# Kernel tuning notes

Hardware: AMD Instinct MI355X
Metric: run time of the kernel (lower is better)

## Reference

```python
import jax, jax.numpy as jnp
import numpy as np

A = 512   # input channels
B = 32    # number of capsule types
H4 = 16   # h*h pose dims per capsule


def setup_inputs() -> dict:
    key = jax.random.key(0)
    k1, k2, k3, k4, k5 = jax.random.split(key, 5)
    # Input feature map [N, A, H, W]
    x = jax.random.normal(k1, (64, A, 32, 32), dtype=jnp.float32)
    # Fused weights: B parallel 1x1 convs concatenated along out-channel dim.
    # Pose convs: B x Conv2d(A -> 16, k=1) -> [B*16, A]; activation convs: B x Conv2d(A -> 1) -> [B, A]
    bound = 1.0 / np.sqrt(A)  # PyTorch Conv2d default init range
    W_pose = jax.random.uniform(k2, (B * H4, A), minval=-bound, maxval=bound, dtype=jnp.float32)
    b_pose = jax.random.uniform(k3, (B * H4,), minval=-bound, maxval=bound, dtype=jnp.float32)
    W_act = jax.random.uniform(k4, (B, A), minval=-bound, maxval=bound, dtype=jnp.float32)
    b_act = jax.random.uniform(k5, (B,), minval=-bound, maxval=bound, dtype=jnp.float32)
    return {"x": x, "W_pose": W_pose, "b_pose": b_pose, "W_act": W_act, "b_act": b_act}


def reference(x, W_pose, b_pose, W_act, b_act):
    # 1x1 conv == channel contraction; fuse all 2*B tiny convs into two GEMMs.
    # poses: [N, B*16, H, W]
    poses = jnp.einsum('nahw,oa->nohw', x, W_pose) + b_pose[None, :, None, None]
    # activations: sigmoid([N, B, H, W])
    activations = jax.nn.sigmoid(jnp.einsum('nahw,oa->nohw', x, W_act) + b_act[None, :, None, None])
    return poses, activations
```

## Files before the change

kernel.cpp:

```cpp
#include <hip/hip_runtime.h>
#include <hip/hip_bf16.h>


typedef __attribute__((ext_vector_type(8))) short short8;
typedef __attribute__((ext_vector_type(4))) float f32x4;

#define A_CH   512
#define HW     1024
#define N_B    64
#define O_POSE 512
#define O_ACT  32
#define O_TOT  544
#define O_PAD  640
#define TO     128
#define TM     128
#define BK     32
#define NIT    (A_CH / BK)

__device__ __forceinline__ unsigned pk(float lo, float hi) {
    __hip_bfloat162 h = __float22bfloat162_rn(make_float2(lo, hi));
    return *reinterpret_cast<unsigned*>(&h);
}

__device__ __forceinline__ void glds16(const void* g, void* l) {
    __builtin_amdgcn_global_load_lds(
        (const __attribute__((address_space(1))) unsigned*)g,
        (__attribute__((address_space(3))) unsigned*)l, 16, 0, 0);
}

__global__ __launch_bounds__(256) void prep_w(const float* __restrict__ Wp,
                                              const float* __restrict__ Wa,
                                              unsigned short* __restrict__ Wb) {
    const int r = blockIdx.x;
    const int c = threadIdx.x * 2;
    float2 v = make_float2(0.f, 0.f);
    if (r < O_POSE)     v = *(const float2*)(Wp + (size_t)r * A_CH + c);
    else if (r < O_TOT) v = *(const float2*)(Wa + (size_t)(r - O_POSE) * A_CH + c);
    __hip_bfloat162 h = __float22bfloat162_rn(v);
    *(unsigned*)(Wb + (size_t)r * A_CH + c) = *reinterpret_cast<unsigned*>(&h);
}

__global__ __launch_bounds__(512, 4) void caps_gemm(
    const float* __restrict__ x,
    const unsigned short* __restrict__ Wb,
    const float* __restrict__ bp,
    const float* __restrict__ ba,
    float* __restrict__ out)
{
    __shared__ __align__(16) short ldsA[3][TO * BK];
    __shared__ __align__(16) short ldsB[2][TM * BK];

    const int tid = threadIdx.x;

    const int lin  = blockIdx.x;
    const int xcd  = lin & 7;
    const int slot = lin >> 3;
    const int ob   = slot % 5;
    const int mnid = (slot / 5) * 8 + xcd;
    const int m0   = (mnid & 7) * TM;
    const int n    = mnid >> 3;
    const int o0   = ob * TO;

    const unsigned short* asrc =
        Wb + (size_t)(o0 + (tid >> 2)) * A_CH + (((tid & 3) ^ ((tid >> 3) & 3)) * 8);

    const int sm = tid & 127;
    const int kg = tid >> 7;
    const float* sbase = x + (size_t)n * A_CH * HW + m0 + sm + (size_t)(kg * 8) * HW;
    const int xwr = sm * BK + ((kg ^ ((sm >> 1) & 3)) * 8);

    float xr[2][8];

    const int lane = tid & 63;
    const int w    = tid >> 6;
    const int wo   = (w >> 2) * 64;
    const int wm   = (w & 3) * 32;
    const int l16  = lane & 15;
    const int g    = lane >> 4;

    f32x4 acc[4][2] = {};

    glds16(asrc, &ldsA[0][tid * 8]);
#pragma unroll
    for (int j = 0; j < 8; ++j) xr[0][j] = sbase[(size_t)j * HW];
    asm volatile("" ::: "memory");
    glds16(asrc + BK, &ldsA[1][tid * 8]);
#pragma unroll
    for (int j = 0; j < 8; ++j) xr[1][j] = sbase[(size_t)(BK + j) * HW];

    asm volatile("s_waitcnt vmcnt(9)" ::: "memory");
    {
        short8 v;
#pragma unroll
        for (int j = 0; j < 4; ++j)
            ((unsigned*)&v)[j] = pk(xr[0][2 * j], xr[0][2 * j + 1]);
        *(short8*)&ldsB[0][xwr] = v;
    }
    asm volatile("s_waitcnt lgkmcnt(0)\n\ts_barrier" ::: "memory");

#pragma unroll
    for (int it = 0; it < NIT; ++it) {
        if (it + 2 < NIT) {
            glds16(asrc + (it + 2) * BK, &ldsA[(it + 2) % 3][tid * 8]);
#pragma unroll
            for (int j = 0; j < 8; ++j)
                xr[it & 1][j] = sbase[(size_t)((it + 2) * BK + j) * HW];
        }
        short8 aF[4], bF[2];
#pragma unroll
        for (int f = 0; f < 4; ++f) {
            const int r = wo + f * 16 + l16;
            aF[f] = *(const short8*)&ldsA[it % 3][r * BK + ((g ^ ((r >> 1) & 3)) * 8)];
        }
#pragma unroll
        for (int f = 0; f < 2; ++f) {
            const int c = wm + f * 16 + l16;
            bF[f] = *(const short8*)&ldsB[it & 1][c * BK + ((g ^ ((c >> 1) & 3)) * 8)];
        }
#pragma unroll
        for (int fo = 0; fo < 4; ++fo)
#pragma unroll
            for (int fm = 0; fm < 2; ++fm)
                acc[fo][fm] = __builtin_amdgcn_mfma_f32_16x16x32_bf16(
                    aF[fo], bF[fm], acc[fo][fm], 0, 0, 0);
        if (it + 1 < NIT) {
            if (it + 2 < NIT)
                asm volatile("s_waitcnt vmcnt(9)" ::: "memory");
            else
                asm volatile("s_waitcnt vmcnt(0)" ::: "memory");
            short8 v;
#pragma unroll
            for (int j = 0; j < 4; ++j)
                ((unsigned*)&v)[j] = pk(xr[(it + 1) & 1][2 * j], xr[(it + 1) & 1][2 * j + 1]);
            *(short8*)&ldsB[(it + 1) & 1][xwr] = v;
            asm volatile("s_waitcnt lgkmcnt(0)\n\ts_barrier" ::: "memory");
        }
    }

    float* actOut = out + (size_t)N_B * O_POSE * HW;
    const size_t poseN = (size_t)n * O_POSE * HW;
    const size_t actN  = (size_t)n * O_ACT * HW;
#pragma unroll
    for (int fo = 0; fo < 4; ++fo) {
#pragma unroll
        for (int i = 0; i < 4; ++i) {
            const int R = o0 + wo + fo * 16 + g * 4 + i;
            if (R >= O_TOT) continue;
            if (R < O_POSE) {
                const float bias = bp[R];
#pragma unroll
                for (int fm = 0; fm < 2; ++fm) {
                    const int cc = m0 + wm + fm * 16 + l16;
                    __builtin_nontemporal_store(acc[fo][fm][i] + bias,
                                                &out[poseN + (size_t)R * HW + cc]);
                }
            } else {
                const float bias = ba[R - O_POSE];
#pragma unroll
                for (int fm = 0; fm < 2; ++fm) {
                    const int cc = m0 + wm + fm * 16 + l16;
                    const float v = acc[fo][fm][i] + bias;
                    __builtin_nontemporal_store(1.0f / (1.0f + __expf(-v)),
                                                &actOut[actN + (size_t)(R - O_POSE) * HW + cc]);
                }
            }
        }
    }
}

extern "C" void kernel_launch(void* const* d_in, const int* in_sizes, int n_in,
                              void* d_out, int out_size, void* d_ws, size_t ws_size,
                              hipStream_t stream) {
    (void)in_sizes; (void)n_in; (void)out_size; (void)ws_size;
    const float* x  = (const float*)d_in[0];
    const float* Wp = (const float*)d_in[1];
    const float* bp = (const float*)d_in[2];
    const float* Wa = (const float*)d_in[3];
    const float* ba = (const float*)d_in[4];
    unsigned short* Wb = (unsigned short*)d_ws;

    prep_w<<<dim3(O_PAD), dim3(256), 0, stream>>>(Wp, Wa, Wb);
    caps_gemm<<<dim3(8 * 5 * N_B), dim3(512), 0, stream>>>(x, Wb, bp, ba, (float*)d_out);
}
```

Measured before the change: 296.4 us.

## Halve workgroup size with 64x64 warp tiles and double-buffered weight staging

```diff
diff --git a/kernel.cpp b/kernel.cpp
--- a/kernel.cpp
+++ b/kernel.cpp
@@ -40,14 +40,14 @@
     *(unsigned*)(Wb + (size_t)r * A_CH + c) = *reinterpret_cast<unsigned*>(&h);
 }
 
-__global__ __launch_bounds__(512, 4) void caps_gemm(
+__global__ __launch_bounds__(256, 3) void caps_gemm(
     const float* __restrict__ x,
     const unsigned short* __restrict__ Wb,
     const float* __restrict__ bp,
     const float* __restrict__ ba,
     float* __restrict__ out)
 {
-    __shared__ __align__(16) short ldsA[3][TO * BK];
+    __shared__ __align__(16) short ldsA[2][TO * BK];
     __shared__ __align__(16) short ldsB[2][TM * BK];
 
     const int tid = threadIdx.x;
@@ -61,79 +61,106 @@
     const int n    = mnid >> 3;
     const int o0   = ob * TO;
 
-    const unsigned short* asrc =
-        Wb + (size_t)(o0 + (tid >> 2)) * A_CH + (((tid & 3) ^ ((tid >> 3) & 3)) * 8);
-
-    const int sm = tid & 127;
-    const int kg = tid >> 7;
-    const float* sbase = x + (size_t)n * A_CH * HW + m0 + sm + (size_t)(kg * 8) * HW;
-    const int xwr = sm * BK + ((kg ^ ((sm >> 1) & 3)) * 8);
-
-    float xr[2][8];
+    const int arow = tid >> 2;
+    const int aslt = tid & 3;
+    const unsigned short* asrc1 =
+        Wb + (size_t)(o0 + arow) * A_CH + ((aslt ^ ((arow >> 1) & 3)) * 8);
+    const unsigned short* asrc2 = asrc1 + (size_t)64 * A_CH;
+
+    const int sm  = tid & 127;
+    const int kg  = tid >> 7;
+    const float* sbase = x + (size_t)n * A_CH * HW + m0 + sm;
+    const int swz = (sm >> 1) & 3;
+    const int wr0 = sm * BK + (((2 * kg)     ^ swz) * 8);
+    const int wr1 = sm * BK + (((2 * kg + 1) ^ swz) * 8);
+
+    float xr[2][16];
 
     const int lane = tid & 63;
     const int w    = tid >> 6;
-    const int wo   = (w >> 2) * 64;
-    const int wm   = (w & 3) * 32;
+    const int wo   = (w >> 1) * 64;
+    const int wm   = (w & 1) * 64;
     const int l16  = lane & 15;
     const int g    = lane >> 4;
 
-    f32x4 acc[4][2] = {};
-
-    glds16(asrc, &ldsA[0][tid * 8]);
-#pragma unroll
-    for (int j = 0; j < 8; ++j) xr[0][j] = sbase[(size_t)j * HW];
+    const unsigned baseA = (unsigned)(uintptr_t)&ldsA[0][0];
+    const unsigned baseB = (unsigned)(uintptr_t)&ldsB[0][0];
+    unsigned aoff[4], boff[4];
+#pragma unroll
+    for (int f = 0; f < 4; ++f) {
+        const int r = wo + f * 16 + l16;
+        aoff[f] = baseA + (unsigned)(r * BK + ((g ^ ((r >> 1) & 3)) * 8)) * 2u;
+        const int c = wm + f * 16 + l16;
+        boff[f] = baseB + (unsigned)(c * BK + ((g ^ ((c >> 1) & 3)) * 8)) * 2u;
+    }
+
+    f32x4 acc[4][4] = {};
+
+    glds16(asrc1, &ldsA[0][tid * 8]);
+    glds16(asrc2, &ldsA[0][2048 + tid * 8]);
     asm volatile("" ::: "memory");
-    glds16(asrc + BK, &ldsA[1][tid * 8]);
-#pragma unroll
-    for (int j = 0; j < 8; ++j) xr[1][j] = sbase[(size_t)(BK + j) * HW];
-
-    asm volatile("s_waitcnt vmcnt(9)" ::: "memory");
+#pragma unroll
+    for (int j = 0; j < 16; ++j) xr[0][j] = sbase[(size_t)(kg * 16 + j) * HW];
+    asm volatile("" ::: "memory");
+#pragma unroll
+    for (int j = 0; j < 16; ++j) xr[1][j] = sbase[(size_t)(BK + kg * 16 + j) * HW];
+    asm volatile("s_waitcnt vmcnt(16)" ::: "memory");
     {
-        short8 v;
-#pragma unroll
-        for (int j = 0; j < 4; ++j)
-            ((unsigned*)&v)[j] = pk(xr[0][2 * j], xr[0][2 * j + 1]);
-        *(short8*)&ldsB[0][xwr] = v;
-    }
-    asm volatile("s_waitcnt lgkmcnt(0)\n\ts_barrier" ::: "memory");
+        short8 v0, v1;
+#pragma unroll
+        for (int j = 0; j < 4; ++j) {
+            ((unsigned*)&v0)[j] = pk(xr[0][2 * j],     xr[0][2 * j + 1]);
+            ((unsigned*)&v1)[j] = pk(xr[0][8 + 2 * j], xr[0][9 + 2 * j]);
+        }
+        *(short8*)&ldsB[0][wr0] = v0;
+        *(short8*)&ldsB[0][wr1] = v1;
+    }
+    asm volatile("s_waitcnt lgkmcnt(0)\ns_barrier" ::: "memory");
 
 #pragma unroll
     for (int it = 0; it < NIT; ++it) {
+        const int cur = it & 1;
+        if (it + 1 < NIT) {
+            glds16(asrc1 + (it + 1) * BK, &ldsA[cur ^ 1][tid * 8]);
+            glds16(asrc2 + (it + 1) * BK, &ldsA[cur ^ 1][2048 + tid * 8]);
+            asm volatile("" ::: "memory");
+        }
         if (it + 2 < NIT) {
-            glds16(asrc + (it + 2) * BK, &ldsA[(it + 2) % 3][tid * 8]);
-#pragma unroll
-            for (int j = 0; j < 8; ++j)
-                xr[it & 1][j] = sbase[(size_t)((it + 2) * BK + j) * HW];
-        }
-        short8 aF[4], bF[2];
-#pragma unroll
-        for (int f = 0; f < 4; ++f) {
-            const int r = wo + f * 16 + l16;
-            aF[f] = *(const short8*)&ldsA[it % 3][r * BK + ((g ^ ((r >> 1) & 3)) * 8)];
-        }
-#pragma unroll
-        for (int f = 0; f < 2; ++f) {
-            const int c = wm + f * 16 + l16;
-            bF[f] = *(const short8*)&ldsB[it & 1][c * BK + ((g ^ ((c >> 1) & 3)) * 8)];
-        }
+#pragma unroll
+            for (int j = 0; j < 16; ++j)
+                xr[cur][j] = sbase[(size_t)((it + 2) * BK + kg * 16 + j) * HW];
+        }
+        short8 aF[4], bF[4];
+#pragma unroll
+        for (int f = 0; f < 4; ++f)
+            asm volatile("ds_read_b128 %0, %1" : "=v"(aF[f]) : "v"(aoff[f] + cur * 8192u));
+#pragma unroll
+        for (int f = 0; f < 4; ++f)
+            asm volatile("ds_read_b128 %0, %1" : "=v"(bF[f]) : "v"(boff[f] + cur * 8192u));
+        asm volatile("s_waitcnt lgkmcnt(0)" ::: "memory");
+        __builtin_amdgcn_sched_barrier(0);
 #pragma unroll
         for (int fo = 0; fo < 4; ++fo)
 #pragma unroll
-            for (int fm = 0; fm < 2; ++fm)
+            for (int fm = 0; fm < 4; ++fm)
                 acc[fo][fm] = __builtin_amdgcn_mfma_f32_16x16x32_bf16(
                     aF[fo], bF[fm], acc[fo][fm], 0, 0, 0);
         if (it + 1 < NIT) {
+            if (it + 2 < NIT) asm volatile("s_waitcnt vmcnt(18)" ::: "memory");
+            else              asm volatile("s_waitcnt vmcnt(2)"  ::: "memory");
+            const int b = cur ^ 1;
+            short8 v0, v1;
+#pragma unroll
+            for (int j = 0; j < 4; ++j) {
+                ((unsigned*)&v0)[j] = pk(xr[b][2 * j],     xr[b][2 * j + 1]);
+                ((unsigned*)&v1)[j] = pk(xr[b][8 + 2 * j], xr[b][9 + 2 * j]);
+            }
+            *(short8*)&ldsB[b][wr0] = v0;
+            *(short8*)&ldsB[b][wr1] = v1;
             if (it + 2 < NIT)
-                asm volatile("s_waitcnt vmcnt(9)" ::: "memory");
+                asm volatile("s_waitcnt vmcnt(16) lgkmcnt(0)\ns_barrier" ::: "memory");
             else
-                asm volatile("s_waitcnt vmcnt(0)" ::: "memory");
-            short8 v;
-#pragma unroll
-            for (int j = 0; j < 4; ++j)
-                ((unsigned*)&v)[j] = pk(xr[(it + 1) & 1][2 * j], xr[(it + 1) & 1][2 * j + 1]);
-            *(short8*)&ldsB[(it + 1) & 1][xwr] = v;
-            asm volatile("s_waitcnt lgkmcnt(0)\n\ts_barrier" ::: "memory");
+                asm volatile("s_waitcnt vmcnt(0) lgkmcnt(0)\ns_barrier" ::: "memory");
         }
     }
 
@@ -149,7 +176,7 @@
             if (R < O_POSE) {
                 const float bias = bp[R];
 #pragma unroll
-                for (int fm = 0; fm < 2; ++fm) {
+                for (int fm = 0; fm < 4; ++fm) {
                     const int cc = m0 + wm + fm * 16 + l16;
                     __builtin_nontemporal_store(acc[fo][fm][i] + bias,
                                                 &out[poseN + (size_t)R * HW + cc]);
@@ -157,7 +184,7 @@
             } else {
                 const float bias = ba[R - O_POSE];
 #pragma unroll
-                for (int fm = 0; fm < 2; ++fm) {
+                for (int fm = 0; fm < 4; ++fm) {
                     const int cc = m0 + wm + fm * 16 + l16;
                     const float v = acc[fo][fm][i] + bias;
                     __builtin_nontemporal_store(1.0f / (1.0f + __expf(-v)),
@@ -180,5 +207,5 @@
     unsigned short* Wb = (unsigned short*)d_ws;
 
     prep_w<<<dim3(O_PAD), dim3(256), 0, stream>>>(Wp, Wa, Wb);
-    caps_gemm<<<dim3(8 * 5 * N_B), dim3(512), 0, stream>>>(x, Wb, bp, ba, (float*)d_out);
-}
+    caps_gemm<<<dim3(8 * 5 * N_B), dim3(256), 0, stream>>>(x, Wb, bp, ba, (float*)d_out);
+}
```

Measured after the change: 297.1 us. No clear change (+0.2%).
